# Kernel optimization log

Measured on AMD Instinct MI355X. Metric: run time of the kernel, lower is better.

The kernel has to match this reference:

```python
import jax, jax.numpy as jnp
import numpy as np
from functools import partial

H = 51  # hidden size hard-coded in the module


def _lstm_cell(x, h, c, W_ih, b_ih, W_hh, b_hh):
    # PyTorch LSTMCell gate order: i, f, g, o stacked along dim 0 of W (4H rows)
    gates = x @ W_ih.T + b_ih + h @ W_hh.T + b_hh  # [B, 4H]
    i, f, g, o = jnp.split(gates, 4, axis=-1)
    i = jax.nn.sigmoid(i)
    f = jax.nn.sigmoid(f)
    g = jnp.tanh(g)
    o = jax.nn.sigmoid(o)
    c_new = f * c + i * g
    h_new = o * jnp.tanh(c_new)
    return h_new, c_new


def setup_inputs() -> dict:
    key = jax.random.key(0)
    ks = jax.random.split(key, 11)
    B, T = 2048, 512
    bound = 1.0 / np.sqrt(H)  # torch LSTMCell/Linear default init: U(-1/sqrt(H), 1/sqrt(H))
    u = lambda k, shape: jax.random.uniform(k, shape, jnp.float32, -bound, bound)
    return {
        "x": jax.random.normal(ks[0], (B, T), dtype=jnp.float32),
        "future": 0,
        "W_ih1": u(ks[1], (4 * H, 1)),
        "b_ih1": u(ks[2], (4 * H,)),
        "W_hh1": u(ks[3], (4 * H, H)),
        "b_hh1": u(ks[4], (4 * H,)),
        "W_ih2": u(ks[5], (4 * H, H)),
        "b_ih2": u(ks[6], (4 * H,)),
        "W_hh2": u(ks[7], (4 * H, H)),
        "b_hh2": u(ks[8], (4 * H,)),
        "fc_w": u(ks[9], (1, H)),
        "fc_b": u(ks[10], (1,)),
    }


def reference(x, future, W_ih1, b_ih1, W_hh1, b_hh1,
              W_ih2, b_ih2, W_hh2, b_hh2, fc_w, fc_b):
    B = x.shape[0]
    z = jnp.zeros((B, H), dtype=x.dtype)

    def cell_stack(x_t, carry):
        h1, c1, h2, c2 = carry
        h1, c1 = _lstm_cell(x_t, h1, c1, W_ih1, b_ih1, W_hh1, b_hh1)
        h2, c2 = _lstm_cell(h1, h2, c2, W_ih2, b_ih2, W_hh2, b_hh2)
        out = h2 @ fc_w.T + fc_b  # [B, 1]
        return (h1, c1, h2, c2), out

    def step(carry, x_t):
        return cell_stack(x_t, carry)

    xs = jnp.swapaxes(x, 0, 1)[:, :, None]  # [T, B, 1]
    carry, outs = jax.lax.scan(step, (z, z, z, z), xs)  # outs: [T, B, 1]
    outputs = jnp.swapaxes(outs[:, :, 0], 0, 1)  # [B, T]

    if future > 0:
        last = outs[-1]  # [B, 1]

        def fstep(c, _):
            inner, out = c
            inner, out = cell_stack(out, inner)
            return (inner, out), out

        _, fouts = jax.lax.scan(fstep, (carry, last), None, length=future)
        outputs = jnp.concatenate([outputs, jnp.swapaxes(fouts[:, :, 0], 0, 1)], axis=1)

    return outputs
```

## Files before the change

### kernel.cpp

```cpp
#include <hip/hip_runtime.h>

#define HID   51
#define T_LEN 512
#define BT    8
#define NTH   832

#define X_OFF   0
#define OUT_OFF 4128
#define H1_OFF  8256
#define H2_OFF  9280

#define L2E 1.4426950408889634f

typedef _Float16 h8 __attribute__((ext_vector_type(8)));
typedef float    f4 __attribute__((ext_vector_type(4)));

__device__ __forceinline__ float fast_rcp(float x) { return __builtin_amdgcn_rcpf(x); }

#if __has_builtin(__builtin_amdgcn_exp2f)
__device__ __forceinline__ float exp2_f(float x) { return __builtin_amdgcn_exp2f(x); }
#else
__device__ __forceinline__ float exp2_f(float x) { return exp2f(x); }
#endif

__device__ __forceinline__ float sigm2(float X) { return fast_rcp(1.0f + exp2_f(-X)); }
__device__ __forceinline__ float tanh2(float E) {
    return fmaf(-2.0f, fast_rcp(exp2_f(E) + 1.0f), 1.0f);
}

__device__ __forceinline__ float dpp_ror8(float v) {
    int t = __builtin_amdgcn_update_dpp(0, __float_as_int(v), 0x128, 0xf, 0xf, true);
    return __int_as_float(t);
}

__device__ __forceinline__ h8 cvt_frag1(const float* p) {
    float4 a = *(const float4*)p;
    float4 b = *(const float4*)(p + 4);
    h8 h;
    h[0] = (_Float16)a.x; h[1] = (_Float16)a.y; h[2] = (_Float16)a.z; h[3] = (_Float16)a.w;
    h[4] = (_Float16)b.x; h[5] = (_Float16)b.y; h[6] = (_Float16)b.z; h[7] = (_Float16)b.w;
    return h;
}

__device__ __forceinline__ float gate_update(const float G[4], float& c) {
    float iv = sigm2(G[0]);
    float fv = sigm2(G[1]);
    float gv = tanh2(G[2]);
    float ov = sigm2(G[3]);
    c = fmaf(fv, c, iv * gv);
    return ov * tanh2(c * (2.0f * L2E));
}

#define MFMA16(A, B, C) __builtin_amdgcn_mfma_f32_16x16x32_f16((A), (B), (C), 0, 0, 0)

__global__ __launch_bounds__(NTH)
void lstm_seq_kernel(const float* __restrict__ x,
                     const float* __restrict__ W_ih1, const float* __restrict__ b_ih1,
                     const float* __restrict__ W_hh1, const float* __restrict__ b_hh1,
                     const float* __restrict__ W_ih2, const float* __restrict__ b_ih2,
                     const float* __restrict__ W_hh2, const float* __restrict__ b_hh2,
                     const float* __restrict__ fc_w,  const float* __restrict__ fc_b,
                     float* __restrict__ out)
{
    __shared__ __align__(16) float sb[13312];

    const int tid   = threadIdx.x;
    const int b0    = blockIdx.x * BT;
    const int w     = tid >> 6;
    const int lane  = tid & 63;
    const int row16 = lane & 15;
    const int q4    = lane >> 4;
    const int col   = row16;

    h8 a1f[2];
    h8 a2f[4];

    for (int i = tid; i < 208 * 64; i += NTH) {
        int rp = i >> 6, k = i & 63;
        int j = rp >> 2, g = rp & 3;
        float sc = (g == 2) ? 2.0f * L2E : L2E;
        float v = 0.0f;
        if (j < HID) {
            if (k < HID)           v = W_hh1[(g * HID + j) * HID + k] * sc;
            else if (k == HID)     v = W_ih1[g * HID + j] * sc;
            else if (k == HID + 1) v = (b_ih1[g * HID + j] + b_hh1[g * HID + j]) * sc;
        }
        sb[i] = v;
    }
    __syncthreads();
    #pragma unroll
    for (int kt = 0; kt < 2; ++kt)
        a1f[kt] = cvt_frag1(sb + (w * 16 + row16) * 64 + kt * 32 + q4 * 8);
    __syncthreads();

    for (int i = tid; i < 208 * 64; i += NTH) {
        int rp = i >> 6, k = i & 63;
        int j = rp >> 2, g = rp & 3;
        float sc = (g == 2) ? 2.0f * L2E : L2E;
        float v = 0.0f;
        if (j < HID) {
            if (k < HID)           v = W_ih2[(g * HID + j) * HID + k] * sc;
            else if (k == HID + 1) v = (b_ih2[g * HID + j] + b_hh2[g * HID + j]) * sc;
        }
        sb[i] = v;
    }
    __syncthreads();
    #pragma unroll
    for (int kt = 0; kt < 2; ++kt)
        a2f[kt] = cvt_frag1(sb + (w * 16 + row16) * 64 + kt * 32 + q4 * 8);
    __syncthreads();

    for (int i = tid; i < 208 * 64; i += NTH) {
        int rp = i >> 6, k = i & 63;
        int j = rp >> 2, g = rp & 3;
        float sc = (g == 2) ? 2.0f * L2E : L2E;
        float v = 0.0f;
        if (k < HID) {
            if (j < HID)        v = W_hh2[(g * HID + j) * HID + k] * sc;
            else if (rp == 204) v = fc_w[k];
        }
        sb[i] = v;
    }
    __syncthreads();
    #pragma unroll
    for (int kt = 0; kt < 2; ++kt)
        a2f[kt + 2] = cvt_frag1(sb + (w * 16 + row16) * 64 + kt * 32 + q4 * 8);
    __syncthreads();

    const int jq = 4 * w + q4;
    const bool lay1 = (col < 8);
    const int  bsel = col & 7;
    const bool val  = (jq < HID);
    const int offh  = (lay1 ? H1_OFF : H2_OFF) * 2
                    + (jq >> 5) * 512 + ((((jq & 31) >> 3) << 4) + bsel) * 8 + (jq & 7);
    const bool xw = (jq == HID) && lay1;

    float* xl   = sb + X_OFF;
    float* outl = sb + OUT_OFF;
    for (int i = tid; i < BT * 516; i += NTH) {
        int b = i / 516, t = i - 516 * b;
        xl[i] = (t < T_LEN) ? x[(size_t)(b0 + b) * T_LEN + t] : 0.0f;
    }
    for (int i = tid; i < 2048; i += NTH) {
        int w32 = 0;
        if (i < 1024) {
            int r = i & 511;
            int d = r - 386;
            if (d >= 0 && d < 32 && (d & 3) == 0) w32 = 0x00003C00;
        }
        ((int*)(sb + H1_OFF))[i] = w32;
    }

    float c = 0.f;
    const float fcb = fc_b[0];
    const bool outlane = (w == 12) && (q4 == 3) && (col < 8);
    const float* xq  = xl + bsel * 516;
    const float* rA0 = sb + H1_OFF + lane * 4;
    const float* rB0 = sb + H2_OFF + lane * 4;
    _Float16* hwp = (_Float16*)sb + offh;
    const f4 z4 = {0.f, 0.f, 0.f, 0.f};
    __syncthreads();

    if (lay1) {
        if (val) {
            float xv = xq[0];
            float G[4];
            #pragma unroll
            for (int g = 0; g < 4; ++g) {
                float sc = (g == 2) ? 2.0f * L2E : L2E;
                float bs = b_ih1[g * HID + jq] + b_hh1[g * HID + jq];
                G[g] = sc * fmaf(W_ih1[g * HID + jq], xv, bs);
            }
            float hv = gate_update(G, c);
            hwp[0] = (_Float16)hv;
        } else if (xw) {
            hwp[0] = (_Float16)xq[1];
        }
    }
    __syncthreads();

    auto body = [&](int i, int p) {
        const float* rA = rA0 + p * 512;
        const float* rB = rB0 + p * 512;
        h8 bh0 = *(const h8*)(rA);       h8 bh1 = *(const h8*)(rA + 256);
        h8 ch2 = *(const h8*)(rB);       h8 ch3 = *(const h8*)(rB + 256);

        if (xw) hwp[(p ^ 1) * 1024] = (_Float16)xq[i + 2];

        f4 s   = MFMA16(a1f[0], bh0, z4);
        s      = MFMA16(a1f[1], bh1, s);
        f4 u01 = MFMA16(a2f[0], bh0, z4);
        u01    = MFMA16(a2f[1], bh1, u01);
        f4 u23 = MFMA16(a2f[2], ch2, z4);
        u23    = MFMA16(a2f[3], ch3, u23);
        f4 u   = u01 + u23;

        float fcv = u[0];
        float G[4];
        #pragma unroll
        for (int g = 0; g < 4; ++g) {
            float ur = dpp_ror8(u[g]);
            G[g] = lay1 ? s[g] : ur;
        }
        float hv = gate_update(G, c);
        if (val) hwp[(p ^ 1) * 1024] = (_Float16)hv;
        if (outlane && i >= 1) outl[col * 516 + (i - 1)] = fcb + fcv;
        __syncthreads();
    };
    for (int i = 0; i < T_LEN; i += 2) {
        body(i, 0);
        body(i + 1, 1);
    }
    body(T_LEN, 0);

    for (int i = tid; i < BT * T_LEN; i += NTH) {
        int b = i >> 9, tt = i & (T_LEN - 1);
        out[(size_t)(b0 + b) * T_LEN + tt] = outl[b * 516 + tt];
    }
}

extern "C" void kernel_launch(void* const* d_in, const int* in_sizes, int n_in,
                              void* d_out, int out_size, void* d_ws, size_t ws_size,
                              hipStream_t stream) {
    const float* x      = (const float*)d_in[0];
    const float* W_ih1  = (const float*)d_in[2];
    const float* b_ih1v = (const float*)d_in[3];
    const float* W_hh1  = (const float*)d_in[4];
    const float* b_hh1v = (const float*)d_in[5];
    const float* W_ih2  = (const float*)d_in[6];
    const float* b_ih2v = (const float*)d_in[7];
    const float* W_hh2  = (const float*)d_in[8];
    const float* b_hh2v = (const float*)d_in[9];
    const float* fc_w   = (const float*)d_in[10];
    const float* fc_b   = (const float*)d_in[11];
    float* out = (float*)d_out;

    dim3 grid(2048 / BT);
    dim3 block(NTH);
    lstm_seq_kernel<<<grid, block, 0, stream>>>(x, W_ih1, b_ih1v, W_hh1, b_hh1v,
                                                W_ih2, b_ih2v, W_hh2, b_hh2v,
                                                fc_w, fc_b, out);
}
```

Measured before the change: 377.3 us.

## Fold 13 wave tiles onto 8 waves with two tiles per wave

The block shrinks from 13 waves to 8, and waves 0-4 now each handle two 16-row gate tiles. The MFMAs for both tiles are interleaved to hide their latency. The goal is to cut the cost of the per-timestep block barrier, which scales with wave count, and to fill the matrix pipes better per wave. In exchange the critical path per step grows for the waves holding two tiles, those waves need more registers, and the load is uneven across waves.

```diff
diff --git a/kernel.cpp b/kernel.cpp
--- a/kernel.cpp
+++ b/kernel.cpp
@@ -3,7 +3,7 @@
 #define HID   51
 #define T_LEN 512
 #define BT    8
-#define NTH   832
+#define NTH   512
 
 #define X_OFF   0
 #define OUT_OFF 4128
@@ -40,6 +40,13 @@
     h[0] = (_Float16)a.x; h[1] = (_Float16)a.y; h[2] = (_Float16)a.z; h[3] = (_Float16)a.w;
     h[4] = (_Float16)b.x; h[5] = (_Float16)b.y; h[6] = (_Float16)b.z; h[7] = (_Float16)b.w;
     return h;
+}
+
+__device__ __forceinline__ h8 h8_zero() {
+    h8 z;
+    #pragma unroll
+    for (int t = 0; t < 8; ++t) z[t] = (_Float16)0.0f;
+    return z;
 }
 
 __device__ __forceinline__ float gate_update(const float G[4], float& c) {
@@ -72,8 +79,12 @@
     const int q4    = lane >> 4;
     const int col   = row16;
 
-    h8 a1f[2];
-    h8 a2f[4];
+    const int  tA   = w;
+    const int  tB   = w + 8;
+    const bool has2 = (tB < 13);
+
+    h8 a1fA[2], a2fA[4];
+    h8 a1fB[2], a2fB[4];
 
     for (int i = tid; i < 208 * 64; i += NTH) {
         int rp = i >> 6, k = i & 63;
@@ -89,8 +100,11 @@
     }
     __syncthreads();
     #pragma unroll
-    for (int kt = 0; kt < 2; ++kt)
-        a1f[kt] = cvt_frag1(sb + (w * 16 + row16) * 64 + kt * 32 + q4 * 8);
+    for (int kt = 0; kt < 2; ++kt) {
+        a1fA[kt] = cvt_frag1(sb + (tA * 16 + row16) * 64 + kt * 32 + q4 * 8);
+        a1fB[kt] = has2 ? cvt_frag1(sb + (tB * 16 + row16) * 64 + kt * 32 + q4 * 8)
+                        : h8_zero();
+    }
     __syncthreads();
 
     for (int i = tid; i < 208 * 64; i += NTH) {
@@ -106,8 +120,11 @@
     }
     __syncthreads();
     #pragma unroll
-    for (int kt = 0; kt < 2; ++kt)
-        a2f[kt] = cvt_frag1(sb + (w * 16 + row16) * 64 + kt * 32 + q4 * 8);
+    for (int kt = 0; kt < 2; ++kt) {
+        a2fA[kt] = cvt_frag1(sb + (tA * 16 + row16) * 64 + kt * 32 + q4 * 8);
+        a2fB[kt] = has2 ? cvt_frag1(sb + (tB * 16 + row16) * 64 + kt * 32 + q4 * 8)
+                        : h8_zero();
+    }
     __syncthreads();
 
     for (int i = tid; i < 208 * 64; i += NTH) {
@@ -123,17 +140,23 @@
     }
     __syncthreads();
     #pragma unroll
-    for (int kt = 0; kt < 2; ++kt)
-        a2f[kt + 2] = cvt_frag1(sb + (w * 16 + row16) * 64 + kt * 32 + q4 * 8);
-    __syncthreads();
-
-    const int jq = 4 * w + q4;
+    for (int kt = 0; kt < 2; ++kt) {
+        a2fA[kt + 2] = cvt_frag1(sb + (tA * 16 + row16) * 64 + kt * 32 + q4 * 8);
+        a2fB[kt + 2] = has2 ? cvt_frag1(sb + (tB * 16 + row16) * 64 + kt * 32 + q4 * 8)
+                            : h8_zero();
+    }
+    __syncthreads();
+
+    const int jqA = 4 * tA + q4;
+    const int jqB = 4 * tB + q4;
     const bool lay1 = (col < 8);
     const int  bsel = col & 7;
-    const bool val  = (jq < HID);
-    const int offh  = (lay1 ? H1_OFF : H2_OFF) * 2
-                    + (jq >> 5) * 512 + ((((jq & 31) >> 3) << 4) + bsel) * 8 + (jq & 7);
-    const bool xw = (jq == HID) && lay1;
+    const bool valB = (jqB < HID);
+    const int offhA = (lay1 ? H1_OFF : H2_OFF) * 2
+                    + (jqA >> 5) * 512 + ((((jqA & 31) >> 3) << 4) + bsel) * 8 + (jqA & 7);
+    const int offhB = (lay1 ? H1_OFF : H2_OFF) * 2
+                    + (jqB >> 5) * 512 + ((((jqB & 31) >> 3) << 4) + bsel) * 8 + (jqB & 7);
+    const bool xwB = (jqB == HID) && lay1;
 
     float* xl   = sb + X_OFF;
     float* outl = sb + OUT_OFF;
@@ -151,30 +174,43 @@
         ((int*)(sb + H1_OFF))[i] = w32;
     }
 
-    float c = 0.f;
+    float cA = 0.f, cB = 0.f;
     const float fcb = fc_b[0];
-    const bool outlane = (w == 12) && (q4 == 3) && (col < 8);
+    const bool outlaneB = (w == 4) && (q4 == 3) && (col < 8);
     const float* xq  = xl + bsel * 516;
     const float* rA0 = sb + H1_OFF + lane * 4;
     const float* rB0 = sb + H2_OFF + lane * 4;
-    _Float16* hwp = (_Float16*)sb + offh;
+    _Float16* hwpA = (_Float16*)sb + offhA;
+    _Float16* hwpB = (_Float16*)sb + offhB;
     const f4 z4 = {0.f, 0.f, 0.f, 0.f};
     __syncthreads();
 
     if (lay1) {
-        if (val) {
+        {
             float xv = xq[0];
             float G[4];
             #pragma unroll
             for (int g = 0; g < 4; ++g) {
                 float sc = (g == 2) ? 2.0f * L2E : L2E;
-                float bs = b_ih1[g * HID + jq] + b_hh1[g * HID + jq];
-                G[g] = sc * fmaf(W_ih1[g * HID + jq], xv, bs);
-            }
-            float hv = gate_update(G, c);
-            hwp[0] = (_Float16)hv;
-        } else if (xw) {
-            hwp[0] = (_Float16)xq[1];
+                float bs = b_ih1[g * HID + jqA] + b_hh1[g * HID + jqA];
+                G[g] = sc * fmaf(W_ih1[g * HID + jqA], xv, bs);
+            }
+            float hv = gate_update(G, cA);
+            hwpA[0] = (_Float16)hv;
+        }
+        if (valB) {
+            float xv = xq[0];
+            float G[4];
+            #pragma unroll
+            for (int g = 0; g < 4; ++g) {
+                float sc = (g == 2) ? 2.0f * L2E : L2E;
+                float bs = b_ih1[g * HID + jqB] + b_hh1[g * HID + jqB];
+                G[g] = sc * fmaf(W_ih1[g * HID + jqB], xv, bs);
+            }
+            float hv = gate_update(G, cB);
+            hwpB[0] = (_Float16)hv;
+        } else if (xwB) {
+            hwpB[0] = (_Float16)xq[1];
         }
     }
     __syncthreads();
@@ -185,26 +221,45 @@
         h8 bh0 = *(const h8*)(rA);       h8 bh1 = *(const h8*)(rA + 256);
         h8 ch2 = *(const h8*)(rB);       h8 ch3 = *(const h8*)(rB + 256);
 
-        if (xw) hwp[(p ^ 1) * 1024] = (_Float16)xq[i + 2];
-
-        f4 s   = MFMA16(a1f[0], bh0, z4);
-        s      = MFMA16(a1f[1], bh1, s);
-        f4 u01 = MFMA16(a2f[0], bh0, z4);
-        u01    = MFMA16(a2f[1], bh1, u01);
-        f4 u23 = MFMA16(a2f[2], ch2, z4);
-        u23    = MFMA16(a2f[3], ch3, u23);
-        f4 u   = u01 + u23;
-
-        float fcv = u[0];
-        float G[4];
-        #pragma unroll
-        for (int g = 0; g < 4; ++g) {
-            float ur = dpp_ror8(u[g]);
-            G[g] = lay1 ? s[g] : ur;
-        }
-        float hv = gate_update(G, c);
-        if (val) hwp[(p ^ 1) * 1024] = (_Float16)hv;
-        if (outlane && i >= 1) outl[col * 516 + (i - 1)] = fcb + fcv;
+        if (xwB) hwpB[(p ^ 1) * 1024] = (_Float16)xq[i + 2];
+
+        f4 sA = MFMA16(a1fA[0], bh0, z4);
+        f4 sB = MFMA16(a1fB[0], bh0, z4);
+        f4 uA = MFMA16(a2fA[0], bh0, z4);
+        f4 uB = MFMA16(a2fB[0], bh0, z4);
+        sA = MFMA16(a1fA[1], bh1, sA);
+        sB = MFMA16(a1fB[1], bh1, sB);
+        uA = MFMA16(a2fA[1], bh1, uA);
+        uB = MFMA16(a2fB[1], bh1, uB);
+        f4 vA = MFMA16(a2fA[2], ch2, z4);
+        f4 vB = MFMA16(a2fB[2], ch2, z4);
+        vA = MFMA16(a2fA[3], ch3, vA);
+        vB = MFMA16(a2fB[3], ch3, vB);
+        uA = uA + vA;
+        uB = uB + vB;
+
+        {
+            float G[4];
+            #pragma unroll
+            for (int g = 0; g < 4; ++g) {
+                float ur = dpp_ror8(uA[g]);
+                G[g] = lay1 ? sA[g] : ur;
+            }
+            float hv = gate_update(G, cA);
+            hwpA[(p ^ 1) * 1024] = (_Float16)hv;
+        }
+        if (has2) {
+            float fcv = uB[0];
+            float G[4];
+            #pragma unroll
+            for (int g = 0; g < 4; ++g) {
+                float ur = dpp_ror8(uB[g]);
+                G[g] = lay1 ? sB[g] : ur;
+            }
+            float hv = gate_update(G, cB);
+            if (valB) hwpB[(p ^ 1) * 1024] = (_Float16)hv;
+            if (outlaneB && i >= 1) outl[col * 516 + (i - 1)] = fcb + fcv;
+        }
         __syncthreads();
     };
     for (int i = 0; i < T_LEN; i += 2) {
```

Result: slower. 400.5 us (+6.2%).
